# Kernel tuning notes

Hardware: AMD Instinct MI355X
Metric: run time of the kernel (lower is better)

The kernel has to match this reference:

```python
import jax, jax.numpy as jnp
import numpy as np
from jax import lax

B, T, D, H, L = 16, 256, 128, 128, 4  # batch, seq, input_size, hidden, num_layers
NUM_CLASSES = 10
EPS = 1e-5


def instancenorm(x):
    # x: [B, T, C]; InstanceNorm1d normalizes over the length dim (T) per (B, C),
    # biased variance, eps=1e-5, no affine.
    m = x.mean(axis=1, keepdims=True)
    v = x.var(axis=1, keepdims=True)
    return (x - m) / jnp.sqrt(v + EPS)


def lstm_stack(x, Wih, Whh, bih, bhh):
    # x: [B, T, I]; Wih/Whh: [L, 4H, I_or_H]; bih/bhh: [L, 4H]. Gate order i,f,g,o.
    batch = x.shape[0]
    hid = Whh.shape[-1]
    out = x
    for l in range(Wih.shape[0]):
        wih, whh, b = Wih[l], Whh[l], bih[l] + bhh[l]
        h0 = jnp.zeros((batch, hid), dtype=x.dtype)
        c0 = jnp.zeros((batch, hid), dtype=x.dtype)
        xs = out.swapaxes(0, 1)  # [T, B, I]

        def step(carry, xt):
            h, c = carry
            g = xt @ wih.T + h @ whh.T + b
            i, f, gg, o = jnp.split(g, 4, axis=-1)
            c_new = jax.nn.sigmoid(f) * c + jax.nn.sigmoid(i) * jnp.tanh(gg)
            h_new = jax.nn.sigmoid(o) * jnp.tanh(c_new)
            return (h_new, c_new), h_new

        _, hs = lax.scan(step, (h0, c0), xs)
        out = hs.swapaxes(0, 1)  # [B, T, H]
    return out


def setup_inputs() -> dict:
    key = jax.random.key(0)
    ks = jax.random.split(key, 16)
    s = 1.0 / np.sqrt(H)
    u = lambda k, shape: jax.random.uniform(k, shape, jnp.float32, -s, s)
    return {
        "x": jax.random.normal(ks[0], (B, T, D), jnp.float32),
        "Wih": u(ks[1], (L, 4 * H, D)),   # input_size == hidden_size so shapes stack
        "Whh": u(ks[2], (L, 4 * H, H)),
        "bih": u(ks[3], (L, 4 * H)),
        "bhh": u(ks[4], (L, 4 * H)),
        "proj_h_w": u(ks[5], (H, H)),
        "proj_h_b": u(ks[6], (H,)),
        "proj_x_w": u(ks[7], (H, D)),
        "proj_x_b": u(ks[8], (H,)),
        "attn_w": u(ks[9], (H,)),
        "fc_w": u(ks[10], (NUM_CLASSES, H)),
        "fc_b": u(ks[11], (NUM_CLASSES,)),
    }


def reference(x, Wih, Whh, bih, bhh, proj_h_w, proj_h_b, proj_x_w, proj_x_b, attn_w, fc_w, fc_b):
    batch, seq_len, input_dim = x.shape
    # normalize(): means/stdev are detached; torch std is unbiased (ddof=1)
    means = lax.stop_gradient(x.mean(axis=(0, 1), keepdims=True))
    stdev = lax.stop_gradient(x.std(axis=(0, 1), ddof=1, keepdims=True) + EPS)
    x = (x - means) / stdev
    x = instancenorm(x)

    lstm_out = lstm_stack(x, Wih, Whh, bih, bhh)   # dropout is identity in eval
    lstm_out = instancenorm(lstm_out)

    ph = lstm_out @ proj_h_w.T + proj_h_b           # [B, T, H]
    px = x @ proj_x_w.T + proj_x_b                  # [B, T, H]
    px = instancenorm(px)

    # additive attention over expanded [B, T, D, H] (values identical across D,
    # matching the original broadcast/expand semantics)
    combined = jnp.tanh(
        jnp.broadcast_to((ph + px)[:, :, None, :], (batch, seq_len, input_dim, ph.shape[-1]))
    )
    logits = jnp.einsum("btdh,h->btd", combined, attn_w)       # [B, T, D]
    alpha = jax.nn.softmax(logits.reshape(batch, -1), axis=1)   # softmax over T*D
    attention_map = alpha.reshape(batch, seq_len, input_dim)

    # classify: context = sum over (T, D) of lstm_out_ex * alpha
    context = jnp.einsum("bth,btd->bh", ph, attention_map)      # [B, H]
    out = context @ fc_w.T + fc_b                               # [B, num_classes]
    return out, attention_map
```

## Files before the change

kernel.cpp:

```cpp
#include <hip/hip_runtime.h>
#include <math.h>
#include <cstddef>

#define B_ 16
#define T_ 256
#define D_ 128
#define H_ 128
#define L_ 4
#define G_ 512
#define NC_ 10
#define EPS_ 1e-5f
#define C_ 16
#define NCHUNK_ (T_ / C_)

#define HROW_ 144
#define HOFF(k) ((k) + (((k) >> 5) << 2))

typedef float f4v __attribute__((ext_vector_type(4)));

#define LOAD_W8(w, base)                                                   \
    asm volatile(                                                          \
        "global_load_dwordx4 %0, %8, off\n\t"                             \
        "global_load_dwordx4 %1, %8, off offset:16\n\t"                   \
        "global_load_dwordx4 %2, %8, off offset:32\n\t"                   \
        "global_load_dwordx4 %3, %8, off offset:48\n\t"                   \
        "global_load_dwordx4 %4, %8, off offset:64\n\t"                   \
        "global_load_dwordx4 %5, %8, off offset:80\n\t"                   \
        "global_load_dwordx4 %6, %8, off offset:96\n\t"                   \
        "global_load_dwordx4 %7, %8, off offset:112\n\t"                  \
        "s_waitcnt vmcnt(0)"                                               \
        : "=&v"(w[0]), "=&v"(w[1]), "=&v"(w[2]), "=&v"(w[3]),              \
          "=&v"(w[4]), "=&v"(w[5]), "=&v"(w[6]), "=&v"(w[7])               \
        : "v"(base)                                                        \
        : "memory")

#define DOT32R(dst_, warr_, hvarr_)                                        \
    {                                                                      \
        float d0_ = 0.f, d1_ = 0.f;                                        \
        _Pragma("unroll")                                                  \
        for (int j_ = 0; j_ < 8; j_++) {                                   \
            d0_ = fmaf(warr_[j_].x, hvarr_[j_].x, d0_);                    \
            d1_ = fmaf(warr_[j_].y, hvarr_[j_].y, d1_);                    \
            d0_ = fmaf(warr_[j_].z, hvarr_[j_].z, d0_);                    \
            d1_ = fmaf(warr_[j_].w, hvarr_[j_].w, d1_);                    \
        }                                                                  \
        dst_ = d0_ + d1_;                                                  \
    }

__device__ __forceinline__ float sigmoid_(float x) {
    x = fminf(fmaxf(x, -30.f), 30.f);
    return 1.f / (1.f + __expf(-x));
}
__device__ __forceinline__ float tanh_(float x) {
    float ax = fminf(fabsf(x), 15.f);
    float e = __expf(2.f * ax);
    float t = 1.f - 2.f / (e + 1.f);
    return copysignf(t, x);
}
__device__ __forceinline__ void wait_ge_(int* p, int v) {
    if (__hip_atomic_load(p, __ATOMIC_RELAXED, __HIP_MEMORY_SCOPE_AGENT) < v) {
        do { __builtin_amdgcn_s_sleep(1); }
        while (__hip_atomic_load(p, __ATOMIC_RELAXED, __HIP_MEMORY_SCOPE_AGENT) < v);
    }
    (void)__hip_atomic_load(p, __ATOMIC_ACQUIRE, __HIP_MEMORY_SCOPE_AGENT);
}

__global__ __launch_bounds__(512) void stats_bd(const float* __restrict__ x,
                                                float* __restrict__ sum_bd,
                                                float* __restrict__ sq_bd) {
    int b = blockIdx.x;
    int tid = threadIdx.x;
    int d = tid & 127, r = tid >> 7;
    const float* xb = x + (size_t)b * T_ * D_;
    float s = 0.f, q = 0.f;
    for (int t = r; t < T_; t += 4) {
        float v = xb[t * D_ + d];
        s += v; q += v * v;
    }
    __shared__ float ls[512], lq[512];
    ls[tid] = s; lq[tid] = q;
    __syncthreads();
    if (r == 0) {
        s = ls[d] + ls[d + 128] + ls[d + 256] + ls[d + 384];
        q = lq[d] + lq[d + 128] + lq[d + 256] + lq[d + 384];
        sum_bd[b * 128 + d] = s;
        sq_bd[b * 128 + d] = q;
    }
}

__global__ __launch_bounds__(128) void stats_norm(const float* __restrict__ sum_bd,
                                                  const float* __restrict__ sq_bd,
                                                  float* __restrict__ mu_bd,
                                                  float* __restrict__ invn) {
    int d = threadIdx.x;
    float s = 0.f, q = 0.f;
    for (int b = 0; b < B_; b++) { s += sum_bd[b * 128 + d]; q += sq_bd[b * 128 + d]; }
    float n = (float)(B_ * T_);
    float m = s / n;
    float varu = (q - n * m * m) / (n - 1.f);
    float sd = sqrtf(fmaxf(varu, 0.f)) + EPS_;
    for (int b = 0; b < B_; b++) {
        float mu = sum_bd[b * 128 + d] * (1.f / T_);
        float varT = sq_bd[b * 128 + d] * (1.f / T_) - mu * mu;
        mu_bd[b * 128 + d] = mu;
        invn[b * 128 + d] = rsqrtf(fmaxf(varT, 0.f) + EPS_ * sd * sd);
    }
}

__global__ __attribute__((amdgpu_waves_per_eu(2, 2))) __launch_bounds__(512)
void scan_pipe6(const float* __restrict__ x,
                const float* __restrict__ Wih, const float* __restrict__ Whh,
                const float* __restrict__ bih, const float* __restrict__ bhh,
                const float* __restrict__ proj_x_w, const float* __restrict__ proj_x_b,
                const float* __restrict__ mu_bd, const float* __restrict__ invn,
                float* __restrict__ h_glob,
                float* __restrict__ ring,
                float* __restrict__ px,
                float* __restrict__ mu_px, float* __restrict__ inv_px,
                float* __restrict__ mu_ln, float* __restrict__ inv_ln,
                int* __restrict__ flag_h,
                int* __restrict__ flag_g) {
    const int wg = blockIdx.x;
    const int tid = threadIdx.x;
    __shared__ __align__(16) float shbuf[16 * HROW_];

    if (wg < 64) {
        const int r = tid >> 2, q = tid & 3;
        const int l = wg >> 4, b = wg & 15;
        f4v w0[8], w1[8], w2[8], w3[8];
        const float* wl = Whh + (size_t)l * G_ * 128;
        LOAD_W8(w0, wl + ((size_t)(0 * 128 + r)) * 128 + q * 32);
        LOAD_W8(w1, wl + ((size_t)(1 * 128 + r)) * 128 + q * 32);
        LOAD_W8(w2, wl + ((size_t)(2 * 128 + r)) * 128 + q * 32);
        LOAD_W8(w3, wl + ((size_t)(3 * 128 + r)) * 128 + q * 32);
        float c = 0.f;
        if (tid < HROW_) shbuf[tid] = 0.f;
        const float* rsl = ring + ((size_t)l * 16 + b) * (4 * C_ * G_);
        float* hob = h_glob + ((size_t)l * 16 + b) * T_ * 128;
        int* fg = flag_g + l * 16 + b;
        int* fh = flag_h + l * 16 + b;
        float hreg[C_];
        __syncthreads();

        for (int k = 0; k < NCHUNK_; k++) {
            if (tid == 0) wait_ge_(fg, k + 1);
            __syncthreads();
#pragma unroll
            for (int half = 0; half < 2; half++) {
                float p0[8], p1[8], p2[8], p3[8];
#pragma unroll
                for (int s8 = 0; s8 < 8; s8++) {
                    int s = half * 8 + s8;
                    const float* gp = rsl + ((size_t)(k & 3) * C_ + s) * G_;
                    p0[s8] = __hip_atomic_load(gp + r, __ATOMIC_RELAXED, __HIP_MEMORY_SCOPE_AGENT);
                    p1[s8] = __hip_atomic_load(gp + 128 + r, __ATOMIC_RELAXED, __HIP_MEMORY_SCOPE_AGENT);
                    p2[s8] = __hip_atomic_load(gp + 256 + r, __ATOMIC_RELAXED, __HIP_MEMORY_SCOPE_AGENT);
                    p3[s8] = __hip_atomic_load(gp + 384 + r, __ATOMIC_RELAXED, __HIP_MEMORY_SCOPE_AGENT);
                }
#pragma unroll
                for (int s8 = 0; s8 < 8; s8++) {
                    int s = half * 8 + s8;
                    int t = k * C_ + s;
                    const f4v* hb4 = (const f4v*)(shbuf + (t & 1) * HROW_ + q * 36);
                    f4v hv[8];
#pragma unroll
                    for (int j = 0; j < 8; j++) hv[j] = hb4[j];
                    float zi, zf, zg, zo;
                    DOT32R(zi, w0, hv);
                    DOT32R(zf, w1, hv);
                    DOT32R(zg, w2, hv);
                    DOT32R(zo, w3, hv);
                    zi += __shfl_xor(zi, 1); zi += __shfl_xor(zi, 2);
                    zf += __shfl_xor(zf, 1); zf += __shfl_xor(zf, 2);
                    zg += __shfl_xor(zg, 1); zg += __shfl_xor(zg, 2);
                    zo += __shfl_xor(zo, 1); zo += __shfl_xor(zo, 2);
                    zi += p0[s8]; zf += p1[s8]; zg += p2[s8]; zo += p3[s8];
                    float ai = sigmoid_(zi), af = sigmoid_(zf);
                    float ag = tanh_(zg),    ao = sigmoid_(zo);
                    c = fmaf(af, c, ai * ag);
                    float hn = ao * tanh_(c);
                    if (q == 0) shbuf[((t + 1) & 1) * HROW_ + HOFF(r)] = hn;
                    hreg[s] = hn;
                    __syncthreads();
                }
            }
            if (q == 0) {
#pragma unroll
                for (int s = 0; s < C_; s++)
                    __hip_atomic_store(hob + (size_t)(k * C_ + s) * 128 + r, hreg[s],
                                       __ATOMIC_RELAXED, __HIP_MEMORY_SCOPE_AGENT);
            }
            __syncthreads();
            if (tid == 0) __hip_atomic_store(fh, k + 1, __ATOMIC_RELEASE, __HIP_MEMORY_SCOPE_AGENT);
        }
    } else if (wg < 128) {
        const int r = tid >> 2, q = tid & 3;
        const int l = (wg - 64) >> 4, b = (wg - 64) & 15;
        f4v w0[8], w1[8], w2[8], w3[8];
        const float* wl = Wih + (size_t)l * G_ * 128;
        LOAD_W8(w0, wl + ((size_t)(0 * 128 + r)) * 128 + q * 32);
        LOAD_W8(w1, wl + ((size_t)(1 * 128 + r)) * 128 + q * 32);
        LOAD_W8(w2, wl + ((size_t)(2 * 128 + r)) * 128 + q * 32);
        LOAD_W8(w3, wl + ((size_t)(3 * 128 + r)) * 128 + q * 32);
        float bs0 = bih[l * G_ + r] + bhh[l * G_ + r];
        float bs1 = bih[l * G_ + 128 + r] + bhh[l * G_ + 128 + r];
        float bs2 = bih[l * G_ + 256 + r] + bhh[l * G_ + 256 + r];
        float bs3 = bih[l * G_ + 384 + r] + bhh[l * G_ + 384 + r];
        const float* hsrc = (l > 0) ? h_glob + ((size_t)(l - 1) * 16 + b) * T_ * 128
                                    : x + (size_t)b * T_ * 128;
        float muk = 0.f, ivk = 1.f;
        if (l == 0) { muk = mu_bd[b * 128 + (tid & 127)]; ivk = invn[b * 128 + (tid & 127)]; }
        float* rout = ring + ((size_t)l * 16 + b) * (4 * C_ * G_);
        int* fhp = (l > 0) ? flag_h + (l - 1) * 16 + b : flag_h;
        int* fhme = flag_h + l * 16 + b;
        int* fgo = flag_g + l * 16 + b;

        for (int k = 0; k < NCHUNK_; k++) {
            if (tid == 0) {
                if (l > 0) wait_ge_(fhp, k + 1);
                if (k >= 4) wait_ge_(fhme, k - 3);
            }
            __syncthreads();
#pragma unroll
            for (int i = 0; i < 4; i++) {
                int idx = i * 512 + tid;
                float v;
                if (l == 0) {
                    v = hsrc[(size_t)k * C_ * 128 + idx];
                    v = (v - muk) * ivk;
                } else {
                    v = __hip_atomic_load(hsrc + (size_t)k * C_ * 128 + idx,
                                          __ATOMIC_RELAXED, __HIP_MEMORY_SCOPE_AGENT);
                }
                shbuf[(idx >> 7) * HROW_ + HOFF(idx & 127)] = v;
            }
            __syncthreads();
#pragma unroll
            for (int s = 0; s < C_; s++) {
                const f4v* hb4 = (const f4v*)(shbuf + s * HROW_ + q * 36);
                f4v hv[8];
#pragma unroll
                for (int j = 0; j < 8; j++) hv[j] = hb4[j];
                float z0, z1, z2, z3;
                DOT32R(z0, w0, hv);
                DOT32R(z1, w1, hv);
                DOT32R(z2, w2, hv);
                DOT32R(z3, w3, hv);
                z0 += __shfl_xor(z0, 1); z0 += __shfl_xor(z0, 2);
                z1 += __shfl_xor(z1, 1); z1 += __shfl_xor(z1, 2);
                z2 += __shfl_xor(z2, 1); z2 += __shfl_xor(z2, 2);
                z3 += __shfl_xor(z3, 1); z3 += __shfl_xor(z3, 2);
                if (q == 0) {
                    float* ro = rout + ((size_t)(k & 3) * C_ + s) * G_;
                    __hip_atomic_store(ro + r, z0 + bs0, __ATOMIC_RELAXED, __HIP_MEMORY_SCOPE_AGENT);
                    __hip_atomic_store(ro + 128 + r, z1 + bs1, __ATOMIC_RELAXED, __HIP_MEMORY_SCOPE_AGENT);
                    __hip_atomic_store(ro + 256 + r, z2 + bs2, __ATOMIC_RELAXED, __HIP_MEMORY_SCOPE_AGENT);
                    __hip_atomic_store(ro + 384 + r, z3 + bs3, __ATOMIC_RELAXED, __HIP_MEMORY_SCOPE_AGENT);
                }
            }
            __syncthreads();
            if (tid == 0) __hip_atomic_store(fgo, k + 1, __ATOMIC_RELEASE, __HIP_MEMORY_SCOPE_AGENT);
        }
    } else if (wg < 144) {
        const int b = wg - 128;
        const int h = tid & 127, tq = tid >> 7;
        f4v w0[8], w1[8], w2[8], w3[8];
        LOAD_W8(w0, proj_x_w + (size_t)h * 128 + 0);
        LOAD_W8(w1, proj_x_w + (size_t)h * 128 + 32);
        LOAD_W8(w2, proj_x_w + (size_t)h * 128 + 64);
        LOAD_W8(w3, proj_x_w + (size_t)h * 128 + 96);
        float bsx = proj_x_b[h];
        float muk = mu_bd[b * 128 + h], ivk = invn[b * 128 + h];
        const float* xb = x + (size_t)b * T_ * 128;
        float* pxb = px + (size_t)b * T_ * 128;
        float sacc = 0.f, qacc = 0.f;

        for (int blk = 0; blk < 16; blk++) {
            int t0 = blk * 16;
            __syncthreads();
#pragma unroll
            for (int j = 0; j < 4; j++) {
                int tt = tq * 4 + j;
                float v = xb[(size_t)(t0 + tt) * 128 + h];
                shbuf[tt * HROW_ + HOFF(h)] = (v - muk) * ivk;
            }
            __syncthreads();
#pragma unroll
            for (int j = 0; j < 4; j++) {
                int tt = tq * 4 + j;
                const float* row = shbuf + tt * HROW_;
                f4v hv[8];
                float p0, p1, p2, p3;
                const f4v* r4 = (const f4v*)(row + 0 * 36);
#pragma unroll
                for (int u = 0; u < 8; u++) hv[u] = r4[u];
                DOT32R(p0, w0, hv);
                r4 = (const f4v*)(row + 1 * 36);
#pragma unroll
                for (int u = 0; u < 8; u++) hv[u] = r4[u];
                DOT32R(p1, w1, hv);
                r4 = (const f4v*)(row + 2 * 36);
#pragma unroll
                for (int u = 0; u < 8; u++) hv[u] = r4[u];
                DOT32R(p2, w2, hv);
                r4 = (const f4v*)(row + 3 * 36);
#pragma unroll
                for (int u = 0; u < 8; u++) hv[u] = r4[u];
                DOT32R(p3, w3, hv);
                float val = (p0 + p1) + (p2 + p3) + bsx;
                pxb[(size_t)(t0 + tt) * 128 + h] = val;
                sacc += val; qacc += val * val;
            }
        }
        __syncthreads();
        shbuf[tq * 128 + h] = sacc;
        shbuf[512 + tq * 128 + h] = qacc;
        __syncthreads();
        if (tq == 0) {
            float s = shbuf[h] + shbuf[128 + h] + shbuf[256 + h] + shbuf[384 + h];
            float qq = shbuf[512 + h] + shbuf[640 + h] + shbuf[768 + h] + shbuf[896 + h];
            float m = s * (1.f / T_);
            float v = qq * (1.f / T_) - m * m;
            mu_px[b * 128 + h] = m;
            inv_px[b * 128 + h] = rsqrtf(fmaxf(v, 0.f) + EPS_);
        }
    } else {
        const int b = wg - 144;
        const int h = tid & 127, st = tid >> 7;
        const float* hsrc = h_glob + ((size_t)3 * 16 + b) * T_ * 128;
        int* f3 = flag_h + 3 * 16 + b;
        float s = 0.f, q = 0.f;
        for (int k = 0; k < NCHUNK_; k++) {
            if (tid == 0) wait_ge_(f3, k + 1);
            __syncthreads();
#pragma unroll
            for (int j = 0; j < 4; j++) {
                int tt = st * 4 + j;
                float v = __hip_atomic_load(hsrc + (size_t)(k * C_ + tt) * 128 + h,
                                            __ATOMIC_RELAXED, __HIP_MEMORY_SCOPE_AGENT);
                s += v; q += v * v;
            }
        }
        shbuf[st * 128 + h] = s;
        shbuf[512 + st * 128 + h] = q;
        __syncthreads();
        if (st == 0) {
            float ss = shbuf[h] + shbuf[128 + h] + shbuf[256 + h] + shbuf[384 + h];
            float qq = shbuf[512 + h] + shbuf[640 + h] + shbuf[768 + h] + shbuf[896 + h];
            float m = ss * (1.f / T_);
            float v = qq * (1.f / T_) - m * m;
            mu_ln[b * 128 + h] = m;
            inv_ln[b * 128 + h] = rsqrtf(fmaxf(v, 0.f) + EPS_);
        }
    }
}

__global__ __launch_bounds__(256) void gemm_score(const float* __restrict__ A,
                                                  const float* __restrict__ mu,
                                                  const float* __restrict__ inv,
                                                  const float* __restrict__ Bw,
                                                  const float* __restrict__ b1,
                                                  const float* __restrict__ px,
                                                  const float* __restrict__ mu_px,
                                                  const float* __restrict__ inv_px,
                                                  const float* __restrict__ attn_w,
                                                  float* __restrict__ ph,
                                                  float* __restrict__ lsc) {
    __shared__ __align__(16) float As[16][64];
    __shared__ __align__(16) float Bs[16][128];
    __shared__ float red[64][17];
    int tid = threadIdx.x;
    int m0 = blockIdx.x * 64;
    int lr = tid >> 2, lc = (tid & 3) << 2;
    int lrB = tid >> 1, lcB = (tid & 1) << 3;
    int tr = tid >> 4, tc = tid & 15;
    int tm = tr << 2, tn = tc << 3;
    float acc[4][8] = {};
    int bidx = (m0 + lr) >> 8;
    const float* Arow = A + (size_t)(m0 + lr) * 128 + lc;
    const float* mup = mu + bidx * 128 + lc;
    const float* ivp = inv + bidx * 128 + lc;
    const float* Brow = Bw + (size_t)lrB * 128 + lcB;
    for (int kb = 0; kb < 128; kb += 16) {
        float4 av = *(const float4*)(Arow + kb);
        float4 m4 = *(const float4*)(mup + kb);
        float4 i4 = *(const float4*)(ivp + kb);
        av.x = (av.x - m4.x) * i4.x; av.y = (av.y - m4.y) * i4.y;
        av.z = (av.z - m4.z) * i4.z; av.w = (av.w - m4.w) * i4.w;
        float4 bv0 = *(const float4*)(Brow + kb);
        float4 bv1 = *(const float4*)(Brow + kb + 4);
        __syncthreads();
        As[lc + 0][lr] = av.x; As[lc + 1][lr] = av.y; As[lc + 2][lr] = av.z; As[lc + 3][lr] = av.w;
        Bs[lcB + 0][lrB] = bv0.x; Bs[lcB + 1][lrB] = bv0.y; Bs[lcB + 2][lrB] = bv0.z; Bs[lcB + 3][lrB] = bv0.w;
        Bs[lcB + 4][lrB] = bv1.x; Bs[lcB + 5][lrB] = bv1.y; Bs[lcB + 6][lrB] = bv1.z; Bs[lcB + 7][lrB] = bv1.w;
        __syncthreads();
#pragma unroll
        for (int k = 0; k < 16; k++) {
            float ar[4], br[8];
#pragma unroll
            for (int i = 0; i < 4; i++) ar[i] = As[k][tm + i];
#pragma unroll
            for (int j = 0; j < 8; j++) br[j] = Bs[k][tn + j];
#pragma unroll
            for (int i = 0; i < 4; i++)
#pragma unroll
                for (int j = 0; j < 8; j++)
                    acc[i][j] = fmaf(ar[i], br[j], acc[i][j]);
        }
    }
    float spart[4];
#pragma unroll
    for (int i = 0; i < 4; i++) {
        int row = m0 + tm + i;
        int bb = row >> 8;
        float sp = 0.f;
#pragma unroll
        for (int j = 0; j < 8; j++) {
            int col = tn + j;
            float val = acc[i][j] + b1[col];
            ph[(size_t)row * 128 + col] = val;
            float inx = (px[(size_t)row * 128 + col] - mu_px[bb * 128 + col]) * inv_px[bb * 128 + col];
            sp = fmaf(tanh_(val + inx), attn_w[col], sp);
        }
        spart[i] = sp;
    }
    __syncthreads();
#pragma unroll
    for (int i = 0; i < 4; i++) red[tm + i][tc] = spart[i];
    __syncthreads();
    if (tid < 64) {
        float s = 0.f;
#pragma unroll
        for (int j = 0; j < 16; j++) s += red[tid][j];
        lsc[m0 + tid] = s;
    }
}

__global__ __launch_bounds__(256) void tail3(const float* __restrict__ lsc,
                                             const float* __restrict__ ph,
                                             const float* __restrict__ fc_w,
                                             const float* __restrict__ fc_b,
                                             float* __restrict__ out,
                                             float* __restrict__ out_att) {
    int b = blockIdx.x;
    int tid = threadIdx.x;
    int h = tid & 127, st = tid >> 7;
    const float* phb = ph + (size_t)b * T_ * H_;
    __shared__ float tmp[256], wsh[256], ls[256];
    float v = lsc[b * 256 + tid];
    tmp[tid] = v; __syncthreads();
    for (int off = 128; off > 0; off >>= 1) { if (tid < off) tmp[tid] = fmaxf(tmp[tid], tmp[tid + off]); __syncthreads(); }
    float mx = tmp[0]; __syncthreads();
    float e = __expf(v - mx);
    tmp[tid] = e; __syncthreads();
    for (int off = 128; off > 0; off >>= 1) { if (tid < off) tmp[tid] += tmp[tid + off]; __syncthreads(); }
    wsh[tid] = e / tmp[0];
    __syncthreads();
    {
        float* ob = out_att + (size_t)b * T_ * D_;
        const float invD = 1.f / (float)D_;
        for (int i = tid; i < T_ * D_; i += 256) ob[i] = wsh[i >> 7] * invD;
    }
    {
        float acc = 0.f;
        for (int t = st; t < T_; t += 2) acc = fmaf(phb[t * 128 + h], wsh[t], acc);
        ls[tid] = acc;
        __syncthreads();
        if (tid < 128) ls[tid] = ls[tid] + ls[tid + 128];
        __syncthreads();
        if (tid < NC_) {
            float s = fc_b[tid];
            const float* fw = fc_w + tid * 128;
            for (int k = 0; k < 128; k++) s = fmaf(ls[k], fw[k], s);
            out[b * NC_ + tid] = s;
        }
    }
}

extern "C" void kernel_launch(void* const* d_in, const int* in_sizes, int n_in,
                              void* d_out, int out_size, void* d_ws, size_t ws_size,
                              hipStream_t stream) {
    const float* x        = (const float*)d_in[0];
    const float* Wih      = (const float*)d_in[1];
    const float* Whh      = (const float*)d_in[2];
    const float* bih      = (const float*)d_in[3];
    const float* bhh      = (const float*)d_in[4];
    const float* proj_h_w = (const float*)d_in[5];
    const float* proj_h_b = (const float*)d_in[6];
    const float* proj_x_w = (const float*)d_in[7];
    const float* proj_x_b = (const float*)d_in[8];
    const float* attn_w   = (const float*)d_in[9];
    const float* fc_w     = (const float*)d_in[10];
    const float* fc_b     = (const float*)d_in[11];
    float* out = (float*)d_out;

    float* ws = (float*)d_ws;
    const size_t NTD = (size_t)B_ * T_ * D_;
    float* h_glob = ws;
    float* ring   = h_glob + 4 * NTD;
    float* px     = ring + 4 * NTD;
    float* smalls = px + NTD;
    float* sum_bd = smalls;
    float* sq_bd  = sum_bd + 2048;
    float* mu_bd  = sq_bd + 2048;
    float* invn   = mu_bd + 2048;
    float* mu_ln  = invn + 2048;
    float* inv_ln = mu_ln + 2048;
    float* mu_px  = inv_ln + 2048;
    float* inv_px = mu_px + 2048;
    float* lsc    = inv_px + 2048;
    int*   flags  = (int*)(lsc + 4096);
    int*   flag_h = flags;
    int*   flag_g = flags + 64;
    float* ph = h_glob;
    const float* h3 = h_glob + 3 * NTD;

    hipMemsetAsync((void*)flags, 0, 128 * sizeof(int), stream);

    stats_bd<<<16, 512, 0, stream>>>(x, sum_bd, sq_bd);
    stats_norm<<<1, 128, 0, stream>>>(sum_bd, sq_bd, mu_bd, invn);

    scan_pipe6<<<160, 512, 0, stream>>>(x, Wih, Whh, bih, bhh,
                                        proj_x_w, proj_x_b, mu_bd, invn,
                                        h_glob, ring, px, mu_px, inv_px,
                                        mu_ln, inv_ln, flag_h, flag_g);

    gemm_score<<<64, 256, 0, stream>>>(h3, mu_ln, inv_ln, proj_h_w, proj_h_b,
                                       px, mu_px, inv_px, attn_w, ph, lsc);

    tail3<<<16, 256, 0, stream>>>(lsc, ph, fc_w, fc_b, out, out + B_ * NC_);
}
```

Baseline: 493.3 us.

## Remap LSTM recurrence to 8-lane K-split, split stats and tail across more blocks

The recurrent and input-projection workgroups now give each thread 8 gate rows with a 16-wide K slice, reduced over 8 lanes by shuffles, instead of 4 rows with 32-wide slices over 4 lanes. The shared h buffer gets a new padded layout to match. The statistics kernel is split into 256 strip blocks with a wider final reduction, and the tail kernel spreads the attention-map write over 4 blocks per batch. The aim is a shorter serial dot product on the recurrence critical path and more parallelism in the small kernels, at the cost of extra shuffle rounds and more register pressure per thread.

After: 749.7 us. 1.52x slower.

```diff
diff --git a/kernel.cpp b/kernel.cpp
--- a/kernel.cpp
+++ b/kernel.cpp
@@ -15,8 +15,21 @@
 
 #define HROW_ 144
 #define HOFF(k) ((k) + (((k) >> 5) << 2))
+#define HROWP_ 160
+#define HOFFP(k) ((k) + (((k) >> 4) << 2))
 
 typedef float f4v __attribute__((ext_vector_type(4)));
+
+#define LOAD_W4(w, base)                                                   \
+    asm volatile(                                                          \
+        "global_load_dwordx4 %0, %4, off\n\t"                             \
+        "global_load_dwordx4 %1, %4, off offset:16\n\t"                   \
+        "global_load_dwordx4 %2, %4, off offset:32\n\t"                   \
+        "global_load_dwordx4 %3, %4, off offset:48\n\t"                   \
+        "s_waitcnt vmcnt(0)"                                               \
+        : "=&v"(w[0]), "=&v"(w[1]), "=&v"(w[2]), "=&v"(w[3])               \
+        : "v"(base)                                                        \
+        : "memory")
 
 #define LOAD_W8(w, base)                                                   \
     asm volatile(                                                          \
@@ -34,6 +47,19 @@
         : "v"(base)                                                        \
         : "memory")
 
+#define DOT16R(dst_, warr_, hvarr_)                                        \
+    {                                                                      \
+        float d0_ = 0.f, d1_ = 0.f;                                        \
+        _Pragma("unroll")                                                  \
+        for (int u_ = 0; u_ < 4; u_++) {                                   \
+            d0_ = fmaf(warr_[u_].x, hvarr_[u_].x, d0_);                    \
+            d1_ = fmaf(warr_[u_].y, hvarr_[u_].y, d1_);                    \
+            d0_ = fmaf(warr_[u_].z, hvarr_[u_].z, d0_);                    \
+            d1_ = fmaf(warr_[u_].w, hvarr_[u_].w, d1_);                    \
+        }                                                                  \
+        dst_ = d0_ + d1_;                                                  \
+    }
+
 #define DOT32R(dst_, warr_, hvarr_)                                        \
     {                                                                      \
         float d0_ = 0.f, d1_ = 0.f;                                        \
@@ -66,14 +92,15 @@
 }
 
 __global__ __launch_bounds__(512) void stats_bd(const float* __restrict__ x,
-                                                float* __restrict__ sum_bd,
-                                                float* __restrict__ sq_bd) {
-    int b = blockIdx.x;
+                                                float* __restrict__ psum,
+                                                float* __restrict__ psq) {
+    int blk = blockIdx.x;
+    int b = blk >> 4, strip = blk & 15;
     int tid = threadIdx.x;
     int d = tid & 127, r = tid >> 7;
-    const float* xb = x + (size_t)b * T_ * D_;
+    const float* xb = x + (size_t)b * T_ * D_ + (size_t)strip * 16 * D_;
     float s = 0.f, q = 0.f;
-    for (int t = r; t < T_; t += 4) {
+    for (int t = r; t < 16; t += 4) {
         float v = xb[t * D_ + d];
         s += v; q += v * v;
     }
@@ -83,32 +110,40 @@
     if (r == 0) {
         s = ls[d] + ls[d + 128] + ls[d + 256] + ls[d + 384];
         q = lq[d] + lq[d + 128] + lq[d + 256] + lq[d + 384];
-        sum_bd[b * 128 + d] = s;
-        sq_bd[b * 128 + d] = q;
-    }
-}
-
-__global__ __launch_bounds__(128) void stats_norm(const float* __restrict__ sum_bd,
-                                                  const float* __restrict__ sq_bd,
+        psum[blk * 128 + d] = s;
+        psq[blk * 128 + d] = q;
+    }
+}
+
+__global__ __launch_bounds__(128) void stats_norm(const float* __restrict__ psum,
+                                                  const float* __restrict__ psq,
                                                   float* __restrict__ mu_bd,
                                                   float* __restrict__ invn) {
     int d = threadIdx.x;
-    float s = 0.f, q = 0.f;
-    for (int b = 0; b < B_; b++) { s += sum_bd[b * 128 + d]; q += sq_bd[b * 128 + d]; }
+    float S = 0.f, Q = 0.f;
+    float sb[16], qb[16];
+    for (int b = 0; b < 16; b++) {
+        float s = 0.f, q = 0.f;
+        for (int st = 0; st < 16; st++) {
+            s += psum[(b * 16 + st) * 128 + d];
+            q += psq[(b * 16 + st) * 128 + d];
+        }
+        sb[b] = s; qb[b] = q; S += s; Q += q;
+    }
     float n = (float)(B_ * T_);
-    float m = s / n;
-    float varu = (q - n * m * m) / (n - 1.f);
+    float m = S / n;
+    float varu = (Q - n * m * m) / (n - 1.f);
     float sd = sqrtf(fmaxf(varu, 0.f)) + EPS_;
-    for (int b = 0; b < B_; b++) {
-        float mu = sum_bd[b * 128 + d] * (1.f / T_);
-        float varT = sq_bd[b * 128 + d] * (1.f / T_) - mu * mu;
+    for (int b = 0; b < 16; b++) {
+        float mu = sb[b] * (1.f / T_);
+        float varT = qb[b] * (1.f / T_) - mu * mu;
         mu_bd[b * 128 + d] = mu;
         invn[b * 128 + d] = rsqrtf(fmaxf(varT, 0.f) + EPS_ * sd * sd);
     }
 }
 
 __global__ __attribute__((amdgpu_waves_per_eu(2, 2))) __launch_bounds__(512)
-void scan_pipe6(const float* __restrict__ x,
+void scan_pipe7(const float* __restrict__ x,
                 const float* __restrict__ Wih, const float* __restrict__ Whh,
                 const float* __restrict__ bih, const float* __restrict__ bhh,
                 const float* __restrict__ proj_x_w, const float* __restrict__ proj_x_b,
@@ -122,90 +157,101 @@
                 int* __restrict__ flag_g) {
     const int wg = blockIdx.x;
     const int tid = threadIdx.x;
-    __shared__ __align__(16) float shbuf[16 * HROW_];
+    __shared__ __align__(16) float shbuf[16 * HROWP_];
 
     if (wg < 64) {
-        const int r = tid >> 2, q = tid & 3;
+        const int s = tid & 7, g = tid >> 3;
         const int l = wg >> 4, b = wg & 15;
-        f4v w0[8], w1[8], w2[8], w3[8];
+        f4v w[8][4];
+        int Rj[8];
         const float* wl = Whh + (size_t)l * G_ * 128;
-        LOAD_W8(w0, wl + ((size_t)(0 * 128 + r)) * 128 + q * 32);
-        LOAD_W8(w1, wl + ((size_t)(1 * 128 + r)) * 128 + q * 32);
-        LOAD_W8(w2, wl + ((size_t)(2 * 128 + r)) * 128 + q * 32);
-        LOAD_W8(w3, wl + ((size_t)(3 * 128 + r)) * 128 + q * 32);
-        float c = 0.f;
-        if (tid < HROW_) shbuf[tid] = 0.f;
+#pragma unroll
+        for (int j = 0; j < 8; j++) {
+            Rj[j] = ((j >> 1) << 7) + ((j & 1) << 6) + g;
+            LOAD_W4(w[j], wl + (size_t)Rj[j] * 128 + s * 16);
+        }
+        float c0 = 0.f, c1 = 0.f;
+        if (tid < HROWP_) shbuf[tid] = 0.f;
         const float* rsl = ring + ((size_t)l * 16 + b) * (4 * C_ * G_);
         float* hob = h_glob + ((size_t)l * 16 + b) * T_ * 128;
         int* fg = flag_g + l * 16 + b;
         int* fh = flag_h + l * 16 + b;
-        float hreg[C_];
         __syncthreads();
 
         for (int k = 0; k < NCHUNK_; k++) {
             if (tid == 0) wait_ge_(fg, k + 1);
             __syncthreads();
 #pragma unroll
-            for (int half = 0; half < 2; half++) {
-                float p0[8], p1[8], p2[8], p3[8];
-#pragma unroll
-                for (int s8 = 0; s8 < 8; s8++) {
-                    int s = half * 8 + s8;
-                    const float* gp = rsl + ((size_t)(k & 3) * C_ + s) * G_;
-                    p0[s8] = __hip_atomic_load(gp + r, __ATOMIC_RELAXED, __HIP_MEMORY_SCOPE_AGENT);
-                    p1[s8] = __hip_atomic_load(gp + 128 + r, __ATOMIC_RELAXED, __HIP_MEMORY_SCOPE_AGENT);
-                    p2[s8] = __hip_atomic_load(gp + 256 + r, __ATOMIC_RELAXED, __HIP_MEMORY_SCOPE_AGENT);
-                    p3[s8] = __hip_atomic_load(gp + 384 + r, __ATOMIC_RELAXED, __HIP_MEMORY_SCOPE_AGENT);
+            for (int q4 = 0; q4 < 4; q4++) {
+                float p[8][4];
+                float hr0[4], hr1[4];
+                if (s == 0) {
+#pragma unroll
+                    for (int i = 0; i < 4; i++) {
+                        const float* gp = rsl + ((size_t)(k & 3) * C_ + q4 * 4 + i) * G_;
+#pragma unroll
+                        for (int j = 0; j < 8; j++)
+                            p[j][i] = __hip_atomic_load(gp + Rj[j], __ATOMIC_RELAXED, __HIP_MEMORY_SCOPE_AGENT);
+                    }
                 }
 #pragma unroll
-                for (int s8 = 0; s8 < 8; s8++) {
-                    int s = half * 8 + s8;
-                    int t = k * C_ + s;
-                    const f4v* hb4 = (const f4v*)(shbuf + (t & 1) * HROW_ + q * 36);
-                    f4v hv[8];
-#pragma unroll
-                    for (int j = 0; j < 8; j++) hv[j] = hb4[j];
-                    float zi, zf, zg, zo;
-                    DOT32R(zi, w0, hv);
-                    DOT32R(zf, w1, hv);
-                    DOT32R(zg, w2, hv);
-                    DOT32R(zo, w3, hv);
-                    zi += __shfl_xor(zi, 1); zi += __shfl_xor(zi, 2);
-                    zf += __shfl_xor(zf, 1); zf += __shfl_xor(zf, 2);
-                    zg += __shfl_xor(zg, 1); zg += __shfl_xor(zg, 2);
-                    zo += __shfl_xor(zo, 1); zo += __shfl_xor(zo, 2);
-                    zi += p0[s8]; zf += p1[s8]; zg += p2[s8]; zo += p3[s8];
-                    float ai = sigmoid_(zi), af = sigmoid_(zf);
-                    float ag = tanh_(zg),    ao = sigmoid_(zo);
-                    c = fmaf(af, c, ai * ag);
-                    float hn = ao * tanh_(c);
-                    if (q == 0) shbuf[((t + 1) & 1) * HROW_ + HOFF(r)] = hn;
-                    hreg[s] = hn;
+                for (int i4 = 0; i4 < 4; i4++) {
+                    int t = k * C_ + q4 * 4 + i4;
+                    const f4v* hb4 = (const f4v*)(shbuf + (t & 1) * HROWP_ + s * 20);
+                    f4v hv[4];
+#pragma unroll
+                    for (int u = 0; u < 4; u++) hv[u] = hb4[u];
+                    float z[8];
+#pragma unroll
+                    for (int j = 0; j < 8; j++) {
+                        DOT16R(z[j], w[j], hv);
+                        if (s == 0) z[j] += p[j][i4];
+                        z[j] += __shfl_xor(z[j], 1);
+                        z[j] += __shfl_xor(z[j], 2);
+                        z[j] += __shfl_xor(z[j], 4);
+                    }
+                    float ai0 = sigmoid_(z[0]), ai1 = sigmoid_(z[1]);
+                    float af0 = sigmoid_(z[2]), af1 = sigmoid_(z[3]);
+                    float ag0 = tanh_(z[4]),    ag1 = tanh_(z[5]);
+                    float ao0 = sigmoid_(z[6]), ao1 = sigmoid_(z[7]);
+                    c0 = fmaf(af0, c0, ai0 * ag0);
+                    c1 = fmaf(af1, c1, ai1 * ag1);
+                    float h0 = ao0 * tanh_(c0);
+                    float h1 = ao1 * tanh_(c1);
+                    if (s == 0) {
+                        shbuf[((t + 1) & 1) * HROWP_ + HOFFP(g)] = h0;
+                        shbuf[((t + 1) & 1) * HROWP_ + HOFFP(g + 64)] = h1;
+                        hr0[i4] = h0; hr1[i4] = h1;
+                    }
                     __syncthreads();
                 }
-            }
-            if (q == 0) {
-#pragma unroll
-                for (int s = 0; s < C_; s++)
-                    __hip_atomic_store(hob + (size_t)(k * C_ + s) * 128 + r, hreg[s],
-                                       __ATOMIC_RELAXED, __HIP_MEMORY_SCOPE_AGENT);
+                if (s == 0) {
+#pragma unroll
+                    for (int i = 0; i < 4; i++) {
+                        int t = k * C_ + q4 * 4 + i;
+                        __hip_atomic_store(hob + (size_t)t * 128 + g, hr0[i],
+                                           __ATOMIC_RELAXED, __HIP_MEMORY_SCOPE_AGENT);
+                        __hip_atomic_store(hob + (size_t)t * 128 + 64 + g, hr1[i],
+                                           __ATOMIC_RELAXED, __HIP_MEMORY_SCOPE_AGENT);
+                    }
+                }
             }
             __syncthreads();
             if (tid == 0) __hip_atomic_store(fh, k + 1, __ATOMIC_RELEASE, __HIP_MEMORY_SCOPE_AGENT);
         }
     } else if (wg < 128) {
-        const int r = tid >> 2, q = tid & 3;
+        const int s = tid & 7, g = tid >> 3;
         const int l = (wg - 64) >> 4, b = (wg - 64) & 15;
-        f4v w0[8], w1[8], w2[8], w3[8];
+        f4v w[8][4];
+        int Rj[8];
+        float bs[8];
         const float* wl = Wih + (size_t)l * G_ * 128;
-        LOAD_W8(w0, wl + ((size_t)(0 * 128 + r)) * 128 + q * 32);
-        LOAD_W8(w1, wl + ((size_t)(1 * 128 + r)) * 128 + q * 32);
-        LOAD_W8(w2, wl + ((size_t)(2 * 128 + r)) * 128 + q * 32);
-        LOAD_W8(w3, wl + ((size_t)(3 * 128 + r)) * 128 + q * 32);
-        float bs0 = bih[l * G_ + r] + bhh[l * G_ + r];
-        float bs1 = bih[l * G_ + 128 + r] + bhh[l * G_ + 128 + r];
-        float bs2 = bih[l * G_ + 256 + r] + bhh[l * G_ + 256 + r];
-        float bs3 = bih[l * G_ + 384 + r] + bhh[l * G_ + 384 + r];
+#pragma unroll
+        for (int j = 0; j < 8; j++) {
+            Rj[j] = ((j >> 1) << 7) + ((j & 1) << 6) + g;
+            LOAD_W4(w[j], wl + (size_t)Rj[j] * 128 + s * 16);
+            bs[j] = bih[l * G_ + Rj[j]] + bhh[l * G_ + Rj[j]];
+        }
         const float* hsrc = (l > 0) ? h_glob + ((size_t)(l - 1) * 16 + b) * T_ * 128
                                     : x + (size_t)b * T_ * 128;
         float muk = 0.f, ivk = 1.f;
@@ -224,6 +270,7 @@
 #pragma unroll
             for (int i = 0; i < 4; i++) {
                 int idx = i * 512 + tid;
+                int step = idx >> 7, kk = idx & 127;
                 float v;
                 if (l == 0) {
                     v = hsrc[(size_t)k * C_ * 128 + idx];
@@ -232,30 +279,29 @@
                     v = __hip_atomic_load(hsrc + (size_t)k * C_ * 128 + idx,
                                           __ATOMIC_RELAXED, __HIP_MEMORY_SCOPE_AGENT);
                 }
-                shbuf[(idx >> 7) * HROW_ + HOFF(idx & 127)] = v;
-            }
-            __syncthreads();
-#pragma unroll
-            for (int s = 0; s < C_; s++) {
-                const f4v* hb4 = (const f4v*)(shbuf + s * HROW_ + q * 36);
-                f4v hv[8];
-#pragma unroll
-                for (int j = 0; j < 8; j++) hv[j] = hb4[j];
-                float z0, z1, z2, z3;
-                DOT32R(z0, w0, hv);
-                DOT32R(z1, w1, hv);
-                DOT32R(z2, w2, hv);
-                DOT32R(z3, w3, hv);
-                z0 += __shfl_xor(z0, 1); z0 += __shfl_xor(z0, 2);
-                z1 += __shfl_xor(z1, 1); z1 += __shfl_xor(z1, 2);
-                z2 += __shfl_xor(z2, 1); z2 += __shfl_xor(z2, 2);
-                z3 += __shfl_xor(z3, 1); z3 += __shfl_xor(z3, 2);
-                if (q == 0) {
-                    float* ro = rout + ((size_t)(k & 3) * C_ + s) * G_;
-                    __hip_atomic_store(ro + r, z0 + bs0, __ATOMIC_RELAXED, __HIP_MEMORY_SCOPE_AGENT);
-                    __hip_atomic_store(ro + 128 + r, z1 + bs1, __ATOMIC_RELAXED, __HIP_MEMORY_SCOPE_AGENT);
-                    __hip_atomic_store(ro + 256 + r, z2 + bs2, __ATOMIC_RELAXED, __HIP_MEMORY_SCOPE_AGENT);
-                    __hip_atomic_store(ro + 384 + r, z3 + bs3, __ATOMIC_RELAXED, __HIP_MEMORY_SCOPE_AGENT);
+                shbuf[step * HROWP_ + HOFFP(kk)] = v;
+            }
+            __syncthreads();
+#pragma unroll
+            for (int st = 0; st < C_; st++) {
+                const f4v* hb4 = (const f4v*)(shbuf + st * HROWP_ + s * 20);
+                f4v hv[4];
+#pragma unroll
+                for (int u = 0; u < 4; u++) hv[u] = hb4[u];
+                float z[8];
+#pragma unroll
+                for (int j = 0; j < 8; j++) {
+                    DOT16R(z[j], w[j], hv);
+                    z[j] += __shfl_xor(z[j], 1);
+                    z[j] += __shfl_xor(z[j], 2);
+                    z[j] += __shfl_xor(z[j], 4);
+                }
+                if (s == 0) {
+                    float* ro = rout + ((size_t)(k & 3) * C_ + st) * G_;
+#pragma unroll
+                    for (int j = 0; j < 8; j++)
+                        __hip_atomic_store(ro + Rj[j], z[j] + bs[j],
+                                           __ATOMIC_RELAXED, __HIP_MEMORY_SCOPE_AGENT);
                 }
             }
             __syncthreads();
@@ -436,13 +482,13 @@
     }
 }
 
-__global__ __launch_bounds__(256) void tail3(const float* __restrict__ lsc,
+__global__ __launch_bounds__(256) void tail4(const float* __restrict__ lsc,
                                              const float* __restrict__ ph,
                                              const float* __restrict__ fc_w,
                                              const float* __restrict__ fc_b,
                                              float* __restrict__ out,
                                              float* __restrict__ out_att) {
-    int b = blockIdx.x;
+    int b = blockIdx.x >> 2, qt = blockIdx.x & 3;
     int tid = threadIdx.x;
     int h = tid & 127, st = tid >> 7;
     const float* phb = ph + (size_t)b * T_ * H_;
@@ -459,9 +505,10 @@
     {
         float* ob = out_att + (size_t)b * T_ * D_;
         const float invD = 1.f / (float)D_;
-        for (int i = tid; i < T_ * D_; i += 256) ob[i] = wsh[i >> 7] * invD;
-    }
-    {
+        int base = qt * 64 * 128;
+        for (int i = tid; i < 64 * 128; i += 256) ob[base + i] = wsh[(base + i) >> 7] * invD;
+    }
+    if (qt == 0) {
         float acc = 0.f;
         for (int t = st; t < T_; t += 2) acc = fmaf(phb[t * 128 + h], wsh[t], acc);
         ls[tid] = acc;
@@ -500,9 +547,9 @@
     float* ring   = h_glob + 4 * NTD;
     float* px     = ring + 4 * NTD;
     float* smalls = px + NTD;
-    float* sum_bd = smalls;
-    float* sq_bd  = sum_bd + 2048;
-    float* mu_bd  = sq_bd + 2048;
+    float* psum   = smalls;
+    float* psq    = psum + 32768;
+    float* mu_bd  = psq + 32768;
     float* invn   = mu_bd + 2048;
     float* mu_ln  = invn + 2048;
     float* inv_ln = mu_ln + 2048;
@@ -517,10 +564,10 @@
 
     hipMemsetAsync((void*)flags, 0, 128 * sizeof(int), stream);
 
-    stats_bd<<<16, 512, 0, stream>>>(x, sum_bd, sq_bd);
-    stats_norm<<<1, 128, 0, stream>>>(sum_bd, sq_bd, mu_bd, invn);
-
-    scan_pipe6<<<160, 512, 0, stream>>>(x, Wih, Whh, bih, bhh,
+    stats_bd<<<256, 512, 0, stream>>>(x, psum, psq);
+    stats_norm<<<1, 128, 0, stream>>>(psum, psq, mu_bd, invn);
+
+    scan_pipe7<<<160, 512, 0, stream>>>(x, Wih, Whh, bih, bhh,
                                         proj_x_w, proj_x_b, mu_bd, invn,
                                         h_glob, ring, px, mu_px, inv_px,
                                         mu_ln, inv_ln, flag_h, flag_g);
@@ -528,5 +575,5 @@
     gemm_score<<<64, 256, 0, stream>>>(h3, mu_ln, inv_ln, proj_h_w, proj_h_b,
                                        px, mu_px, inv_px, attn_w, ph, lsc);
 
-    tail3<<<16, 256, 0, stream>>>(lsc, ph, fc_w, fc_b, out, out + B_ * NC_);
-}
+    tail4<<<64, 256, 0, stream>>>(lsc, ph, fc_w, fc_b, out, out + B_ * NC_);
+}
```
